# Performance work log

Hardware: AMD Instinct MI355X
Metric: run time of the kernel (lower is better)

The kernel has to match this reference:

```python
import jax, jax.numpy as jnp
import numpy as np

B = 2048
DIMS = [4096, 8192, 8192, 4096]
SPARSITY = 1e-4


def setup_inputs() -> dict:
    key = jax.random.key(0)
    ks = jax.random.split(key, 10)
    x = jax.random.normal(ks[0], (B, DIMS[0]), dtype=jnp.float32)
    inp = {"x": x}
    for i in range(3):
        fan_in, fan_out = DIMS[i], DIMS[i + 1]
        # xavier_uniform_ for tanh
        limit = float(np.sqrt(6.0 / (fan_in + fan_out)))
        W = jax.random.uniform(ks[1 + 3 * i], (fan_out, fan_in),
                               dtype=jnp.float32, minval=-limit, maxval=limit)
        b = jax.random.uniform(ks[2 + 3 * i], (fan_out,), dtype=jnp.float32,
                               minval=-1.0 / np.sqrt(fan_in), maxval=1.0 / np.sqrt(fan_in))
        m = jax.random.bernoulli(ks[3 + 3 * i], p=SPARSITY, shape=(fan_out, fan_in))
        inp[f"W{i+1}"] = W
        inp[f"b{i+1}"] = b
        inp[f"m{i+1}"] = m
    return inp


def reference(x, W1, b1, m1, W2, b2, m2, W3, b3, m3):
    # Each layer: mask weight, dense linear (y = x @ (W*m)^T + b), tanh except last.
    h = jnp.tanh(x @ (W1 * m1).T + b1)        # [B, 8192]
    h = jnp.tanh(h @ (W2 * m2).T + b2)        # [B, 8192]
    out = h @ (W3 * m3).T + b3                # [B, 4096]
    return out
```

## Files before the change

### kernel.cpp

```cpp
#include <hip/hip_runtime.h>
#include <stdint.h>

#define CAP 32

typedef unsigned int u32x4 __attribute__((ext_vector_type(4)));
typedef _Float16 half8 __attribute__((ext_vector_type(8)));

static constexpr int BATCH = 2048;
static constexpr int D0 = 4096, D1 = 8192, D2 = 8192, D3 = 4096;
static constexpr int RP = 8192;
static constexpr size_t PREFIX_BYTES = 8u << 20;

static constexpr int CHUNK16 = 8192;
static constexpr int MAXC1 = 2048, MAXC2 = 4096, MAXC3 = 2048;

static constexpr size_t OFF_DET   = 0;
static constexpr size_t OFF_REFD2 = 256;
static constexpr size_t OFF_CNT   = OFF_REFD2 + (size_t)RP * 4;
static constexpr size_t ZERO_BYTES= OFF_CNT + 3ull * RP * 4;
static constexpr size_t OFF_TB    = ZERO_BYTES;
static constexpr size_t OFF_RK    = OFF_TB + 2ull * RP * 4;
static constexpr size_t OFF_RW    = OFF_RK + 3ull * RP * CAP * 4;
static constexpr size_t OFF_XT    = OFF_RW + 3ull * RP * CAP * 4;
static constexpr size_t OFF_H1    = OFF_XT + (size_t)D0 * BATCH * 2;
static constexpr size_t OFF_H2    = OFF_H1 + (size_t)D1 * BATCH * 2;
static constexpr size_t WS_BIG    = OFF_H2 + (size_t)D2 * BATCH * 2;

__device__ __forceinline__ u32x4 ntload4(const u32x4* p) {
    return __builtin_nontemporal_load(p);
}

__global__ __launch_bounds__(256) void detect_kernel(const uint8_t* __restrict__ m,
                                                     unsigned* __restrict__ det) {
    const u32x4* p = (const u32x4*)m;
    const int n16 = (int)(PREFIX_BYTES / 16);
    unsigned c123 = 0, c4 = 0;
    for (int i = blockIdx.x * blockDim.x + threadIdx.x; i < n16; i += gridDim.x * blockDim.x) {
        u32x4 q = ntload4(p + i);
        if ((q.x | q.y | q.z | q.w) == 0u) continue;
        unsigned w4[4] = {q.x, q.y, q.z, q.w};
        for (int t = 0; t < 4; ++t) {
            unsigned v = w4[t];
            if (!v) continue;
            for (int bb = 0; bb < 4; ++bb) {
                if ((v >> (8 * bb)) & 0xFFu) {
                    int pm8 = (t * 4 + bb) & 7;
                    if (pm8 & 3) c123++;
                    else if (pm8 == 4) c4++;
                }
            }
        }
    }
    if (c123) atomicAdd(&det[0], c123);
    if (c4)   atomicAdd(&det[1], c4);
}

__device__ __forceinline__ int decide_mode(const unsigned* det) {
    unsigned c123 = det[0], c4 = det[1];
    if (c123 > 520u) return 0;
    if (c123 > 200u) return 1;
    return (c4 > 40u) ? 1 : 2;
}

__device__ __forceinline__ int esize_of(int mode) { return mode == 0 ? 1 : (mode == 1 ? 4 : 8); }

__device__ __forceinline__ void scat(int e, int flog2, const float* W,
                                     int* cnt, int* rk, float* rw, int* mark) {
    int row = e >> flog2;
    int col = e & ((1 << flog2) - 1);
    int pos = atomicAdd(&cnt[row], 1);
    if (pos < CAP) {
        rk[(size_t)row * CAP + pos] = col;
        rw[(size_t)row * CAP + pos] = __builtin_nontemporal_load(&W[(size_t)e]);
    }
    if (mark) atomicOr(&mark[col], 1);
}

template<int FLOG2>
__device__ __forceinline__ void scan_chunk(const void* __restrict__ mask, const float* __restrict__ W,
                                           int chunk, int mode,
                                           int* cnt, int* rk, float* rw, int* mark) {
    const u32x4* q4 = (const u32x4*)mask;
    const int base16 = chunk * CHUNK16;
    #pragma unroll 1
    for (int it = 0; it < 2; ++it) {
        const u32x4* p = q4 + base16 + it * 4096 + threadIdx.x;
        u32x4 v[16];
        #pragma unroll
        for (int t = 0; t < 16; ++t) v[t] = ntload4(p + t * 256);
        #pragma unroll
        for (int t = 0; t < 16; ++t) {
            u32x4 q = v[t];
            if ((q.x | q.y | q.z | q.w) == 0u) continue;
            int i16 = base16 + it * 4096 + t * 256 + (int)threadIdx.x;
            if (mode == 1) {
                int eb = i16 << 2;
                if (q.x) scat(eb + 0, FLOG2, W, cnt, rk, rw, mark);
                if (q.y) scat(eb + 1, FLOG2, W, cnt, rk, rw, mark);
                if (q.z) scat(eb + 2, FLOG2, W, cnt, rk, rw, mark);
                if (q.w) scat(eb + 3, FLOG2, W, cnt, rk, rw, mark);
            } else if (mode == 0) {
                unsigned w4[4] = {q.x, q.y, q.z, q.w};
                int eb = i16 << 4;
                for (int tt = 0; tt < 4; ++tt) {
                    unsigned x = w4[tt];
                    if (!x) continue;
                    for (int bb = 0; bb < 4; ++bb)
                        if ((x >> (8 * bb)) & 0xFFu)
                            scat(eb + tt * 4 + bb, FLOG2, W, cnt, rk, rw, mark);
                }
            } else {
                int eb = i16 << 1;
                if (q.x | q.y) scat(eb + 0, FLOG2, W, cnt, rk, rw, mark);
                if (q.z | q.w) scat(eb + 1, FLOG2, W, cnt, rk, rw, mark);
            }
        }
    }
}

template<bool HAS_TB, bool USE_REFD>
__device__ __forceinline__ void layer_row(int j, const _Float16* __restrict__ inT,
                                          const float* __restrict__ bias,
                                          const float* __restrict__ tb_in,
                                          const int* __restrict__ cnt_in,
                                          const int* __restrict__ cnt,
                                          const int* __restrict__ rk,
                                          const float* __restrict__ rw,
                                          const int* __restrict__ refd,
                                          _Float16* __restrict__ outT) {
    int c = cnt[j]; if (c > CAP) c = CAP;
    if (c == 0) return;
    if (USE_REFD && refd[j] == 0) return;

    __shared__ int   ci[CAP];
    __shared__ float wv[CAP];
    if (threadIdx.x == 0) {
        for (int a = 0; a < c; ++a) { ci[a] = rk[(size_t)j * CAP + a]; wv[a] = rw[(size_t)j * CAP + a]; }
        for (int a = 1; a < c; ++a) {
            int k = ci[a]; float w = wv[a]; int b = a - 1;
            while (b >= 0 && ci[b] > k) { ci[b + 1] = ci[b]; wv[b + 1] = wv[b]; --b; }
            ci[b + 1] = k; wv[b + 1] = w;
        }
    }
    __syncthreads();

    float base = bias[j];
    if (HAS_TB)
        for (int e = 0; e < c; ++e)
            if (cnt_in[ci[e]] == 0) base += wv[e] * tb_in[ci[e]];

    const int l = threadIdx.x;
    float acc[8];
    #pragma unroll
    for (int i = 0; i < 8; ++i) acc[i] = base;

    for (int e = 0; e < c; ++e) {
        int k = ci[e];
        if (HAS_TB && cnt_in[k] == 0) continue;
        float w = wv[e];
        half8 v = ((const half8*)(inT + (size_t)k * BATCH))[l];
        #pragma unroll
        for (int i = 0; i < 8; ++i) acc[i] += w * (float)v[i];
    }

    half8 o;
    #pragma unroll
    for (int i = 0; i < 8; ++i) o[i] = (_Float16)tanhf(acc[i]);
    ((half8*)(outT + (size_t)j * BATCH))[l] = o;
}

__device__ __forceinline__ void sort_row_global(int j, const int* cnt, int* rk, float* rw) {
    int c = cnt[j]; if (c > CAP) c = CAP;
    if (c <= 1) return;
    int* K = rk + (size_t)j * CAP; float* W_ = rw + (size_t)j * CAP;
    for (int a = 1; a < c; ++a) {
        int k = K[a]; float w = W_[a]; int b = a - 1;
        while (b >= 0 && K[b] > k) { K[b + 1] = K[b]; W_[b + 1] = W_[b]; --b; }
        K[b + 1] = k; W_[b + 1] = w;
    }
}

__global__ __launch_bounds__(256) void k1_kernel(const void* __restrict__ m1, const float* __restrict__ W1,
                          const float* __restrict__ x,
                          const float* __restrict__ b1, const float* __restrict__ b2,
                          const unsigned* __restrict__ det,
                          int* __restrict__ cnt1, int* __restrict__ rk1, float* __restrict__ rw1,
                          float* __restrict__ tb1, float* __restrict__ tb2,
                          _Float16* __restrict__ xT) {
    const int bid = blockIdx.x;
    if (bid < MAXC1) {
        const int mode = decide_mode(det);
        const int nc = (int)(((size_t)D1 * D0 * esize_of(mode)) >> 17);
        if (bid < nc) scan_chunk<12>(m1, W1, bid, mode, cnt1, rk1, rw1, nullptr);
    } else if (bid < MAXC1 + (D0 / 32) * (BATCH / 32)) {
        __shared__ float tile[32][33];
        const int t = bid - MAXC1;
        const int cx = t & 127, ry = t >> 7;
        const int tx = threadIdx.x & 31, ty = threadIdx.x >> 5;
        const int c0 = cx * 32, r0 = ry * 32;
        for (int i = ty; i < 32; i += 8)
            tile[i][tx] = __builtin_nontemporal_load(&x[(size_t)(r0 + i) * D0 + c0 + tx]);
        __syncthreads();
        for (int i = ty; i < 32; i += 8)
            xT[(size_t)(c0 + i) * BATCH + r0 + tx] = (_Float16)tile[tx][i];
    } else {
        int tid = (bid - MAXC1 - (D0 / 32) * (BATCH / 32)) * 256 + threadIdx.x;
        if (tid < D1) tb1[tid] = tanhf(b1[tid]);
        else if (tid < D1 + D2) tb2[tid - D1] = tanhf(b2[tid - D1]);
    }
}

__global__ __launch_bounds__(256) void k2_kernel(const void* __restrict__ m2, const float* __restrict__ W2,
                          const void* __restrict__ m3, const float* __restrict__ W3,
                          const unsigned* __restrict__ det,
                          int* __restrict__ cnt2, int* __restrict__ rk2, float* __restrict__ rw2,
                          int* __restrict__ cnt3, int* __restrict__ rk3, float* __restrict__ rw3,
                          int* __restrict__ refd2,
                          const _Float16* __restrict__ xT, const float* __restrict__ b1,
                          const int* __restrict__ cnt1, const int* __restrict__ rk1,
                          const float* __restrict__ rw1,
                          _Float16* __restrict__ h1T) {
    const int bid = blockIdx.x;
    if (bid < MAXC2) {
        const int mode = decide_mode(det);
        const int nc = (int)(((size_t)D2 * D1 * esize_of(mode)) >> 17);
        if (bid < nc) scan_chunk<13>(m2, W2, bid, mode, cnt2, rk2, rw2, nullptr);
    } else if (bid < MAXC2 + MAXC3) {
        const int mode = decide_mode(det);
        const int nc = (int)(((size_t)D3 * D2 * esize_of(mode)) >> 17);
        const int ch = bid - MAXC2;
        if (ch < nc) scan_chunk<13>(m3, W3, ch, mode, cnt3, rk3, rw3, refd2);
    } else {
        layer_row<false, false>(bid - MAXC2 - MAXC3, xT, b1, nullptr, nullptr,
                                cnt1, rk1, rw1, nullptr, h1T);
    }
}

__global__ __launch_bounds__(256) void k3_kernel(const _Float16* __restrict__ h1T, const float* __restrict__ b2,
                          const float* __restrict__ tb1, const int* __restrict__ cnt1,
                          const int* __restrict__ cnt2, const int* __restrict__ rk2,
                          const float* __restrict__ rw2, const int* __restrict__ refd2,
                          _Float16* __restrict__ h2T,
                          const int* __restrict__ cnt3, int* __restrict__ rk3, float* __restrict__ rw3) {
    const int bid = blockIdx.x;
    if (bid < D2) {
        layer_row<true, true>(bid, h1T, b2, tb1, cnt1, cnt2, rk2, rw2, refd2, h2T);
    } else {
        int j = (bid - D2) * 256 + threadIdx.x;
        if (j < D3) sort_row_global(j, cnt3, rk3, rw3);
    }
}

__global__ void l3t_kernel(const _Float16* __restrict__ h2T,
                           const float* __restrict__ b3, const float* __restrict__ tb2,
                           const int* __restrict__ cnt2,
                           const int* __restrict__ c3, const int* __restrict__ k3,
                           const float* __restrict__ w3,
                           float* __restrict__ out) {
    __shared__ float tile[32][33];
    const int j0 = blockIdx.x * 32, b0 = blockIdx.y * 32;
    const int tx = threadIdx.x, ty = threadIdx.y;

    for (int s = 0; s < 4; ++s) {
        int jl = ty + 8 * s;
        int j = j0 + jl;
        float acc = b3[j];
        int c = c3[j]; if (c > CAP) c = CAP;
        const int* kk = k3 + (size_t)j * CAP;
        const float* ww = w3 + (size_t)j * CAP;
        for (int e = 0; e < c; ++e) {
            int k = kk[e];
            float w = ww[e];
            acc += w * (cnt2[k] ? (float)h2T[(size_t)k * BATCH + b0 + tx] : tb2[k]);
        }
        tile[jl][tx] = acc;
    }
    __syncthreads();
    for (int s = 0; s < 4; ++s) {
        int bl = ty + 8 * s;
        __builtin_nontemporal_store(tile[tx][bl], &out[(size_t)(b0 + bl) * D3 + j0 + tx]);
    }
}

__global__ __launch_bounds__(256) void scan1_kernel(const void* m, const float* W, const unsigned* det,
                                                    int* cnt, int* rk, float* rw) {
    const int mode = decide_mode(det);
    const int nc = (int)(((size_t)D1 * D0 * esize_of(mode)) >> 17);
    if (blockIdx.x < (unsigned)nc) scan_chunk<12>(m, W, blockIdx.x, mode, cnt, rk, rw, nullptr);
}
__global__ __launch_bounds__(256) void scan2_kernel(const void* m, const float* W, const unsigned* det,
                                                    int* cnt, int* rk, float* rw) {
    const int mode = decide_mode(det);
    const int nc = (int)(((size_t)D2 * D1 * esize_of(mode)) >> 17);
    if (blockIdx.x < (unsigned)nc) scan_chunk<13>(m, W, blockIdx.x, mode, cnt, rk, rw, nullptr);
}
__global__ __launch_bounds__(256) void scan3_kernel(const void* m, const float* W, const unsigned* det,
                                                    int* cnt, int* rk, float* rw) {
    const int mode = decide_mode(det);
    const int nc = (int)(((size_t)D3 * D2 * esize_of(mode)) >> 17);
    if (blockIdx.x < (unsigned)nc) scan_chunk<13>(m, W, blockIdx.x, mode, cnt, rk, rw, nullptr);
}
__global__ __launch_bounds__(256) void sortall_kernel(const int* cnt, int* rk, float* rw) {
    int r = blockIdx.x * 256 + threadIdx.x;
    if (r < 3 * RP) sort_row_global(r, cnt, rk, rw);
}

__global__ void out_kernel(const float* __restrict__ x,
                           const float* __restrict__ b1, const float* __restrict__ b2,
                           const float* __restrict__ b3,
                           const int* __restrict__ c1, const int* __restrict__ k1, const float* __restrict__ w1,
                           const int* __restrict__ c2, const int* __restrict__ k2, const float* __restrict__ w2,
                           const int* __restrict__ c3, const int* __restrict__ k3, const float* __restrict__ w3,
                           float* __restrict__ out) {
    int idx = blockIdx.x * blockDim.x + threadIdx.x;
    if (idx >= BATCH * D3) return;
    int b = idx >> 12, j = idx & 4095;
    float acc = b3[j];
    int c = c3[j]; if (c > CAP) c = CAP;
    for (int e = 0; e < c; ++e) {
        int kk2 = k3[(size_t)j * CAP + e];
        float a2 = b2[kk2];
        int cc2 = c2[kk2]; if (cc2 > CAP) cc2 = CAP;
        for (int e2 = 0; e2 < cc2; ++e2) {
            int kk1 = k2[(size_t)kk2 * CAP + e2];
            float a1 = b1[kk1];
            int cc1 = c1[kk1]; if (cc1 > CAP) cc1 = CAP;
            for (int e1 = 0; e1 < cc1; ++e1)
                a1 += w1[(size_t)kk1 * CAP + e1] * x[(size_t)b * D0 + k1[(size_t)kk1 * CAP + e1]];
            a2 += w2[(size_t)kk2 * CAP + e2] * tanhf(a1);
        }
        acc += w3[(size_t)j * CAP + e] * tanhf(a2);
    }
    out[idx] = acc;
}

extern "C" void kernel_launch(void* const* d_in, const int* in_sizes, int n_in,
                              void* d_out, int out_size, void* d_ws, size_t ws_size,
                              hipStream_t stream) {
    const float* x  = (const float*)d_in[0];
    const float* W1 = (const float*)d_in[1];
    const float* b1 = (const float*)d_in[2];
    const void*  m1 = d_in[3];
    const float* W2 = (const float*)d_in[4];
    const float* b2 = (const float*)d_in[5];
    const void*  m2 = d_in[6];
    const float* W3 = (const float*)d_in[7];
    const float* b3 = (const float*)d_in[8];
    const void*  m3 = d_in[9];

    uint8_t* ws = (uint8_t*)d_ws;
    unsigned* det = (unsigned*)(ws + OFF_DET);
    int* refd2 = (int*)(ws + OFF_REFD2);
    int* cnt1 = (int*)(ws + OFF_CNT);
    int* cnt2 = cnt1 + RP;
    int* cnt3 = cnt2 + RP;
    float* tb1 = (float*)(ws + OFF_TB);
    float* tb2 = tb1 + RP;
    int* rk1 = (int*)(ws + OFF_RK);
    int* rk2 = rk1 + (size_t)RP * CAP;
    int* rk3 = rk2 + (size_t)RP * CAP;
    float* rw1 = (float*)(ws + OFF_RW);
    float* rw2 = rw1 + (size_t)RP * CAP;
    float* rw3 = rw2 + (size_t)RP * CAP;
    _Float16* xT  = (_Float16*)(ws + OFF_XT);
    _Float16* h1T = (_Float16*)(ws + OFF_H1);
    _Float16* h2T = (_Float16*)(ws + OFF_H2);

    hipMemsetAsync(ws, 0, ZERO_BYTES, stream);
    detect_kernel<<<1024, 256, 0, stream>>>((const uint8_t*)m1, det);

    if (ws_size >= WS_BIG) {
        const int K1_BLOCKS = MAXC1 + (D0 / 32) * (BATCH / 32) + (D1 + D2) / 256;
        k1_kernel<<<K1_BLOCKS, 256, 0, stream>>>(
            m1, W1, x, b1, b2, det, cnt1, rk1, rw1, tb1, tb2, xT);

        const int K2_BLOCKS = MAXC2 + MAXC3 + D1;
        k2_kernel<<<K2_BLOCKS, 256, 0, stream>>>(
            m2, W2, m3, W3, det,
            cnt2, rk2, rw2, cnt3, rk3, rw3, refd2,
            xT, b1, cnt1, rk1, rw1, h1T);

        k3_kernel<<<D2 + D3 / 256, 256, 0, stream>>>(
            h1T, b2, tb1, cnt1, cnt2, rk2, rw2, refd2, h2T, cnt3, rk3, rw3);

        l3t_kernel<<<dim3(D3 / 32, BATCH / 32), dim3(32, 8), 0, stream>>>(
            h2T, b3, tb2, cnt2, cnt3, rk3, rw3, (float*)d_out);
    } else {
        scan1_kernel<<<MAXC1, 256, 0, stream>>>(m1, W1, det, cnt1, rk1, rw1);
        scan2_kernel<<<MAXC2, 256, 0, stream>>>(m2, W2, det, cnt2, rk2, rw2);
        scan3_kernel<<<MAXC3, 256, 0, stream>>>(m3, W3, det, cnt3, rk3, rw3);
        sortall_kernel<<<3 * RP / 256, 256, 0, stream>>>(cnt1, rk1, rw1);
        out_kernel<<<(BATCH * D3 + 255) / 256, 256, 0, stream>>>(
            x, b1, b2, b3,
            cnt1, rk1, rw1, cnt2, rk2, rw2, cnt3, rk3, rw3,
            (float*)d_out);
    }
}
```

Measured before the change: 169.1 us.

## Fuse layer-2 computation into final output kernel and drop h2 materialization

Removes the separate layer-2 pass that wrote an fp16 h2T buffer for all referenced rows, and instead computes each needed h2 value on the fly inside the final output kernel by walking the sparse row of W2 over h1T. The referenced-row marking (atomicOr on refd2) is dropped from the W3 scan, and k3 becomes a small sort kernel for W2/W3 rows. The mask scan loop is also reshaped into 4 iterations of 8 loads instead of 2 of 16, lowering register pressure. The trade-off is recomputing h2 entries redundantly per output column that references them, with added gather indirection in the final kernel.

After: 174.6 us. +3.3%, slower.

```diff
diff --git a/kernel.cpp b/kernel.cpp
--- a/kernel.cpp
+++ b/kernel.cpp
@@ -15,16 +15,14 @@
 static constexpr int MAXC1 = 2048, MAXC2 = 4096, MAXC3 = 2048;
 
 static constexpr size_t OFF_DET   = 0;
-static constexpr size_t OFF_REFD2 = 256;
-static constexpr size_t OFF_CNT   = OFF_REFD2 + (size_t)RP * 4;
+static constexpr size_t OFF_CNT   = 256;
 static constexpr size_t ZERO_BYTES= OFF_CNT + 3ull * RP * 4;
 static constexpr size_t OFF_TB    = ZERO_BYTES;
 static constexpr size_t OFF_RK    = OFF_TB + 2ull * RP * 4;
 static constexpr size_t OFF_RW    = OFF_RK + 3ull * RP * CAP * 4;
 static constexpr size_t OFF_XT    = OFF_RW + 3ull * RP * CAP * 4;
 static constexpr size_t OFF_H1    = OFF_XT + (size_t)D0 * BATCH * 2;
-static constexpr size_t OFF_H2    = OFF_H1 + (size_t)D1 * BATCH * 2;
-static constexpr size_t WS_BIG    = OFF_H2 + (size_t)D2 * BATCH * 2;
+static constexpr size_t WS_BIG    = OFF_H1 + (size_t)D1 * BATCH * 2;
 
 __device__ __forceinline__ u32x4 ntload4(const u32x4* p) {
     return __builtin_nontemporal_load(p);
@@ -65,7 +63,7 @@
 __device__ __forceinline__ int esize_of(int mode) { return mode == 0 ? 1 : (mode == 1 ? 4 : 8); }
 
 __device__ __forceinline__ void scat(int e, int flog2, const float* W,
-                                     int* cnt, int* rk, float* rw, int* mark) {
+                                     int* cnt, int* rk, float* rw) {
     int row = e >> flog2;
     int col = e & ((1 << flog2) - 1);
     int pos = atomicAdd(&cnt[row], 1);
@@ -73,32 +71,31 @@
         rk[(size_t)row * CAP + pos] = col;
         rw[(size_t)row * CAP + pos] = __builtin_nontemporal_load(&W[(size_t)e]);
     }
-    if (mark) atomicOr(&mark[col], 1);
 }
 
 template<int FLOG2>
 __device__ __forceinline__ void scan_chunk(const void* __restrict__ mask, const float* __restrict__ W,
                                            int chunk, int mode,
-                                           int* cnt, int* rk, float* rw, int* mark) {
+                                           int* cnt, int* rk, float* rw) {
     const u32x4* q4 = (const u32x4*)mask;
     const int base16 = chunk * CHUNK16;
     #pragma unroll 1
-    for (int it = 0; it < 2; ++it) {
-        const u32x4* p = q4 + base16 + it * 4096 + threadIdx.x;
-        u32x4 v[16];
+    for (int it = 0; it < 4; ++it) {
+        const u32x4* p = q4 + base16 + it * 2048 + threadIdx.x;
+        u32x4 v[8];
         #pragma unroll
-        for (int t = 0; t < 16; ++t) v[t] = ntload4(p + t * 256);
+        for (int t = 0; t < 8; ++t) v[t] = ntload4(p + t * 256);
         #pragma unroll
-        for (int t = 0; t < 16; ++t) {
+        for (int t = 0; t < 8; ++t) {
             u32x4 q = v[t];
             if ((q.x | q.y | q.z | q.w) == 0u) continue;
-            int i16 = base16 + it * 4096 + t * 256 + (int)threadIdx.x;
+            int i16 = base16 + it * 2048 + t * 256 + (int)threadIdx.x;
             if (mode == 1) {
                 int eb = i16 << 2;
-                if (q.x) scat(eb + 0, FLOG2, W, cnt, rk, rw, mark);
-                if (q.y) scat(eb + 1, FLOG2, W, cnt, rk, rw, mark);
-                if (q.z) scat(eb + 2, FLOG2, W, cnt, rk, rw, mark);
-                if (q.w) scat(eb + 3, FLOG2, W, cnt, rk, rw, mark);
+                if (q.x) scat(eb + 0, FLOG2, W, cnt, rk, rw);
+                if (q.y) scat(eb + 1, FLOG2, W, cnt, rk, rw);
+                if (q.z) scat(eb + 2, FLOG2, W, cnt, rk, rw);
+                if (q.w) scat(eb + 3, FLOG2, W, cnt, rk, rw);
             } else if (mode == 0) {
                 unsigned w4[4] = {q.x, q.y, q.z, q.w};
                 int eb = i16 << 4;
@@ -107,30 +104,25 @@
                     if (!x) continue;
                     for (int bb = 0; bb < 4; ++bb)
                         if ((x >> (8 * bb)) & 0xFFu)
-                            scat(eb + tt * 4 + bb, FLOG2, W, cnt, rk, rw, mark);
+                            scat(eb + tt * 4 + bb, FLOG2, W, cnt, rk, rw);
                 }
             } else {
                 int eb = i16 << 1;
-                if (q.x | q.y) scat(eb + 0, FLOG2, W, cnt, rk, rw, mark);
-                if (q.z | q.w) scat(eb + 1, FLOG2, W, cnt, rk, rw, mark);
+                if (q.x | q.y) scat(eb + 0, FLOG2, W, cnt, rk, rw);
+                if (q.z | q.w) scat(eb + 1, FLOG2, W, cnt, rk, rw);
             }
         }
     }
 }
 
-template<bool HAS_TB, bool USE_REFD>
-__device__ __forceinline__ void layer_row(int j, const _Float16* __restrict__ inT,
-                                          const float* __restrict__ bias,
-                                          const float* __restrict__ tb_in,
-                                          const int* __restrict__ cnt_in,
-                                          const int* __restrict__ cnt,
-                                          const int* __restrict__ rk,
-                                          const float* __restrict__ rw,
-                                          const int* __restrict__ refd,
-                                          _Float16* __restrict__ outT) {
+__device__ __forceinline__ void layer1_row(int j, const _Float16* __restrict__ xT,
+                                           const float* __restrict__ b1,
+                                           const int* __restrict__ cnt,
+                                           const int* __restrict__ rk,
+                                           const float* __restrict__ rw,
+                                           _Float16* __restrict__ h1T) {
     int c = cnt[j]; if (c > CAP) c = CAP;
     if (c == 0) return;
-    if (USE_REFD && refd[j] == 0) return;
 
     __shared__ int   ci[CAP];
     __shared__ float wv[CAP];
@@ -144,21 +136,15 @@
     }
     __syncthreads();
 
-    float base = bias[j];
-    if (HAS_TB)
-        for (int e = 0; e < c; ++e)
-            if (cnt_in[ci[e]] == 0) base += wv[e] * tb_in[ci[e]];
-
+    const float base = b1[j];
     const int l = threadIdx.x;
     float acc[8];
     #pragma unroll
     for (int i = 0; i < 8; ++i) acc[i] = base;
 
     for (int e = 0; e < c; ++e) {
-        int k = ci[e];
-        if (HAS_TB && cnt_in[k] == 0) continue;
         float w = wv[e];
-        half8 v = ((const half8*)(inT + (size_t)k * BATCH))[l];
+        half8 v = ((const half8*)(xT + (size_t)ci[e] * BATCH))[l];
         #pragma unroll
         for (int i = 0; i < 8; ++i) acc[i] += w * (float)v[i];
     }
@@ -166,7 +152,7 @@
     half8 o;
     #pragma unroll
     for (int i = 0; i < 8; ++i) o[i] = (_Float16)tanhf(acc[i]);
-    ((half8*)(outT + (size_t)j * BATCH))[l] = o;
+    ((half8*)(h1T + (size_t)j * BATCH))[l] = o;
 }
 
 __device__ __forceinline__ void sort_row_global(int j, const int* cnt, int* rk, float* rw) {
@@ -191,7 +177,7 @@
     if (bid < MAXC1) {
         const int mode = decide_mode(det);
         const int nc = (int)(((size_t)D1 * D0 * esize_of(mode)) >> 17);
-        if (bid < nc) scan_chunk<12>(m1, W1, bid, mode, cnt1, rk1, rw1, nullptr);
+        if (bid < nc) scan_chunk<12>(m1, W1, bid, mode, cnt1, rk1, rw1);
     } else if (bid < MAXC1 + (D0 / 32) * (BATCH / 32)) {
         __shared__ float tile[32][33];
         const int t = bid - MAXC1;
@@ -215,7 +201,6 @@
                           const unsigned* __restrict__ det,
                           int* __restrict__ cnt2, int* __restrict__ rk2, float* __restrict__ rw2,
                           int* __restrict__ cnt3, int* __restrict__ rk3, float* __restrict__ rw3,
-                          int* __restrict__ refd2,
                           const _Float16* __restrict__ xT, const float* __restrict__ b1,
                           const int* __restrict__ cnt1, const int* __restrict__ rk1,
                           const float* __restrict__ rw1,
@@ -224,36 +209,31 @@
     if (bid < MAXC2) {
         const int mode = decide_mode(det);
         const int nc = (int)(((size_t)D2 * D1 * esize_of(mode)) >> 17);
-        if (bid < nc) scan_chunk<13>(m2, W2, bid, mode, cnt2, rk2, rw2, nullptr);
+        if (bid < nc) scan_chunk<13>(m2, W2, bid, mode, cnt2, rk2, rw2);
     } else if (bid < MAXC2 + MAXC3) {
         const int mode = decide_mode(det);
         const int nc = (int)(((size_t)D3 * D2 * esize_of(mode)) >> 17);
         const int ch = bid - MAXC2;
-        if (ch < nc) scan_chunk<13>(m3, W3, ch, mode, cnt3, rk3, rw3, refd2);
+        if (ch < nc) scan_chunk<13>(m3, W3, ch, mode, cnt3, rk3, rw3);
     } else {
-        layer_row<false, false>(bid - MAXC2 - MAXC3, xT, b1, nullptr, nullptr,
-                                cnt1, rk1, rw1, nullptr, h1T);
-    }
-}
-
-__global__ __launch_bounds__(256) void k3_kernel(const _Float16* __restrict__ h1T, const float* __restrict__ b2,
-                          const float* __restrict__ tb1, const int* __restrict__ cnt1,
-                          const int* __restrict__ cnt2, const int* __restrict__ rk2,
-                          const float* __restrict__ rw2, const int* __restrict__ refd2,
-                          _Float16* __restrict__ h2T,
-                          const int* __restrict__ cnt3, int* __restrict__ rk3, float* __restrict__ rw3) {
-    const int bid = blockIdx.x;
-    if (bid < D2) {
-        layer_row<true, true>(bid, h1T, b2, tb1, cnt1, cnt2, rk2, rw2, refd2, h2T);
-    } else {
-        int j = (bid - D2) * 256 + threadIdx.x;
-        if (j < D3) sort_row_global(j, cnt3, rk3, rw3);
-    }
-}
-
-__global__ void l3t_kernel(const _Float16* __restrict__ h2T,
-                           const float* __restrict__ b3, const float* __restrict__ tb2,
-                           const int* __restrict__ cnt2,
+        layer1_row(bid - MAXC2 - MAXC3, xT, b1, cnt1, rk1, rw1, h1T);
+    }
+}
+
+__global__ __launch_bounds__(256) void sort23_kernel(const int* __restrict__ cnt2,
+                          int* __restrict__ rk2, float* __restrict__ rw2,
+                          const int* __restrict__ cnt3,
+                          int* __restrict__ rk3, float* __restrict__ rw3) {
+    int r = blockIdx.x * 256 + threadIdx.x;
+    if (r < RP) sort_row_global(r, cnt2, rk2, rw2);
+    else if (r < RP + D3) sort_row_global(r - RP, cnt3, rk3, rw3);
+}
+
+__global__ void l3t_kernel(const _Float16* __restrict__ h1T,
+                           const float* __restrict__ b2, const float* __restrict__ b3,
+                           const float* __restrict__ tb1, const float* __restrict__ tb2,
+                           const int* __restrict__ cnt1, const int* __restrict__ cnt2,
+                           const int* __restrict__ rk2, const float* __restrict__ rw2,
                            const int* __restrict__ c3, const int* __restrict__ k3,
                            const float* __restrict__ w3,
                            float* __restrict__ out) {
@@ -269,9 +249,25 @@
         const int* kk = k3 + (size_t)j * CAP;
         const float* ww = w3 + (size_t)j * CAP;
         for (int e = 0; e < c; ++e) {
-            int k = kk[e];
+            int k2 = kk[e];
             float w = ww[e];
-            acc += w * (cnt2[k] ? (float)h2T[(size_t)k * BATCH + b0 + tx] : tb2[k]);
+            float hv;
+            int c2 = cnt2[k2]; if (c2 > CAP) c2 = CAP;
+            if (c2 == 0) {
+                hv = tb2[k2];
+            } else {
+                float a2 = b2[k2];
+                const int* kk2 = rk2 + (size_t)k2 * CAP;
+                const float* ww2 = rw2 + (size_t)k2 * CAP;
+                for (int e2 = 0; e2 < c2; ++e2) {
+                    int k1 = kk2[e2];
+                    float w2 = ww2[e2];
+                    a2 += w2 * (cnt1[k1] ? (float)h1T[(size_t)k1 * BATCH + b0 + tx]
+                                         : tb1[k1]);
+                }
+                hv = tanhf(a2);
+            }
+            acc += w * hv;
         }
         tile[jl][tx] = acc;
     }
@@ -286,19 +282,19 @@
                                                     int* cnt, int* rk, float* rw) {
     const int mode = decide_mode(det);
     const int nc = (int)(((size_t)D1 * D0 * esize_of(mode)) >> 17);
-    if (blockIdx.x < (unsigned)nc) scan_chunk<12>(m, W, blockIdx.x, mode, cnt, rk, rw, nullptr);
+    if (blockIdx.x < (unsigned)nc) scan_chunk<12>(m, W, blockIdx.x, mode, cnt, rk, rw);
 }
 __global__ __launch_bounds__(256) void scan2_kernel(const void* m, const float* W, const unsigned* det,
                                                     int* cnt, int* rk, float* rw) {
     const int mode = decide_mode(det);
     const int nc = (int)(((size_t)D2 * D1 * esize_of(mode)) >> 17);
-    if (blockIdx.x < (unsigned)nc) scan_chunk<13>(m, W, blockIdx.x, mode, cnt, rk, rw, nullptr);
+    if (blockIdx.x < (unsigned)nc) scan_chunk<13>(m, W, blockIdx.x, mode, cnt, rk, rw);
 }
 __global__ __launch_bounds__(256) void scan3_kernel(const void* m, const float* W, const unsigned* det,
                                                     int* cnt, int* rk, float* rw) {
     const int mode = decide_mode(det);
     const int nc = (int)(((size_t)D3 * D2 * esize_of(mode)) >> 17);
-    if (blockIdx.x < (unsigned)nc) scan_chunk<13>(m, W, blockIdx.x, mode, cnt, rk, rw, nullptr);
+    if (blockIdx.x < (unsigned)nc) scan_chunk<13>(m, W, blockIdx.x, mode, cnt, rk, rw);
 }
 __global__ __launch_bounds__(256) void sortall_kernel(const int* cnt, int* rk, float* rw) {
     int r = blockIdx.x * 256 + threadIdx.x;
@@ -350,7 +346,6 @@
 
     uint8_t* ws = (uint8_t*)d_ws;
     unsigned* det = (unsigned*)(ws + OFF_DET);
-    int* refd2 = (int*)(ws + OFF_REFD2);
     int* cnt1 = (int*)(ws + OFF_CNT);
     int* cnt2 = cnt1 + RP;
     int* cnt3 = cnt2 + RP;
@@ -364,7 +359,6 @@
     float* rw3 = rw2 + (size_t)RP * CAP;
     _Float16* xT  = (_Float16*)(ws + OFF_XT);
     _Float16* h1T = (_Float16*)(ws + OFF_H1);
-    _Float16* h2T = (_Float16*)(ws + OFF_H2);
 
     hipMemsetAsync(ws, 0, ZERO_BYTES, stream);
     detect_kernel<<<1024, 256, 0, stream>>>((const uint8_t*)m1, det);
@@ -377,14 +371,15 @@
         const int K2_BLOCKS = MAXC2 + MAXC3 + D1;
         k2_kernel<<<K2_BLOCKS, 256, 0, stream>>>(
             m2, W2, m3, W3, det,
-            cnt2, rk2, rw2, cnt3, rk3, rw3, refd2,
+            cnt2, rk2, rw2, cnt3, rk3, rw3,
             xT, b1, cnt1, rk1, rw1, h1T);
 
-        k3_kernel<<<D2 + D3 / 256, 256, 0, stream>>>(
-            h1T, b2, tb1, cnt1, cnt2, rk2, rw2, refd2, h2T, cnt3, rk3, rw3);
+        sort23_kernel<<<(RP + D3) / 256, 256, 0, stream>>>(
+            cnt2, rk2, rw2, cnt3, rk3, rw3);
 
         l3t_kernel<<<dim3(D3 / 32, BATCH / 32), dim3(32, 8), 0, stream>>>(
-            h2T, b3, tb2, cnt2, cnt3, rk3, rw3, (float*)d_out);
+            h1T, b2, b3, tb1, tb2, cnt1, cnt2, rk2, rw2,
+            cnt3, rk3, rw3, (float*)d_out);
     } else {
         scan1_kernel<<<MAXC1, 256, 0, stream>>>(m1, W1, det, cnt1, rk1, rw1);
         scan2_kernel<<<MAXC2, 256, 0, stream>>>(m2, W2, det, cnt2, rk2, rw2);
```
